# Optimization experiments

Hardware: AMD Instinct MI355X
Metric: run time of the kernel (lower is better)

The kernel has to match this reference:

```python
import jax, jax.numpy as jnp
import numpy as np

B, H, W, F_HEX, F_GLB = 2, 48, 48, 150, 7
D, NH, L, DF, M = 512, 8, 4, 2048, 128
MAX_W, MAX_H, ATK, REC = 48, 48, 8, 20
S = H * W
DK = D // NH


def _ln(x, g, b):
    m = jnp.mean(x, -1, keepdims=True)
    v = jnp.mean(jnp.square(x - m), -1, keepdims=True)
    return (x - m) * jax.lax.rsqrt(v + 1e-5) * g + b


def _mha(q, k, v, wq, bq, wk, bk, wv, bv, wo, bo, mask=None):
    Bq, Sq, _ = q.shape
    Sk = k.shape[1]
    Q = (q @ wq + bq).reshape(Bq, Sq, NH, DK)
    K = (k @ wk + bk).reshape(Bq, Sk, NH, DK)
    V = (v @ wv + bv).reshape(Bq, Sk, NH, DK)
    s = jnp.einsum('bqhd,bkhd->bhqk', Q, K) / np.float32(np.sqrt(DK))
    if mask is not None:
        s = jnp.where(mask == 0, jnp.float32(-1e9), s)
    a = jax.nn.softmax(s, -1)
    o = jnp.einsum('bhqk,bkhd->bqhd', a, V).reshape(Bq, Sq, D)
    return o @ wo + bo


def setup_inputs():
    key = jax.random.key(0)
    ks = iter(jax.random.split(key, 64))
    w = lambda *sh: jax.random.normal(next(ks), sh, jnp.float32) * 0.02
    z = lambda *sh: jnp.zeros(sh, jnp.float32)
    o = lambda *sh: jnp.ones(sh, jnp.float32)
    return dict(
        map_representation=jax.random.normal(next(ks), (B, H, W, F_HEX), jnp.float32),
        global_features=jax.random.normal(next(ks), (B, F_GLB), jnp.float32),
        memory=jax.random.normal(next(ks), (B, M, D), jnp.float32),
        fog_mask=jax.random.randint(next(ks), (B, H, W), 0, 2, jnp.int32),
        hex_w=w(F_HEX, D), hex_b=z(D), glob_w=w(F_GLB, D), glob_b=z(D),
        mem_wq=w(D, D), mem_bq=z(D), mem_wk=w(D, D), mem_bk=z(D),
        mem_wv=w(D, D), mem_bv=z(D), mem_wo=w(D, D), mem_bo=z(D),
        gate_w=w(2 * D, D), gate_b=z(D),
        mn1_g=o(D), mn1_b=z(D), mn2_g=o(D), mn2_b=z(D),
        lw_q=w(L, D, D), lb_q=z(L, D), lw_k=w(L, D, D), lb_k=z(L, D),
        lw_v=w(L, D, D), lb_v=z(L, D), lw_o=w(L, D, D), lb_o=z(L, D),
        ln1_g=o(L, D), ln1_b=z(L, D), ln2_g=o(L, D), ln2_b=z(L, D),
        ff1_w=w(L, D, DF), ff1_b=z(L, DF), ff2_w=w(L, DF, D), ff2_b=z(L, D),
        pool_w=w(D, 1), pool_b=z(1),
        sx_w=w(D, MAX_W), sx_b=z(MAX_W), sy_w=w(D, MAX_H), sy_b=z(MAX_H),
        tx_w=w(D, MAX_W), tx_b=z(MAX_W), ty_w=w(D, MAX_H), ty_b=z(MAX_H),
        atk_w=w(D, ATK), atk_b=z(ATK), rec_w=w(D, REC), rec_b=z(REC),
        et_w=w(D, 1), et_b=z(1), val_w=w(D, 1), val_b=z(1),
    )


def reference(map_representation, global_features, memory, fog_mask,
              hex_w, hex_b, glob_w, glob_b,
              mem_wq, mem_bq, mem_wk, mem_bk, mem_wv, mem_bv, mem_wo, mem_bo,
              gate_w, gate_b, mn1_g, mn1_b, mn2_g, mn2_b,
              lw_q, lb_q, lw_k, lb_k, lw_v, lb_v, lw_o, lb_o,
              ln1_g, ln1_b, ln2_g, ln2_b, ff1_w, ff1_b, ff2_w, ff2_b,
              pool_w, pool_b, sx_w, sx_b, sy_w, sy_b, tx_w, tx_b, ty_w, ty_b,
              atk_w, atk_b, rec_w, rec_b, et_w, et_b, val_w, val_b):
    # project hex + global features, flatten map to token sequence [B,S,D]
    hexf = map_representation @ hex_w + hex_b
    glob = global_features @ glob_w + glob_b
    seq = (hexf + glob[:, None, None, :]).reshape(B, S, D)
    am = fog_mask.reshape(B, S)[:, None, None, :]  # key mask [B,1,1,S]

    # memory module: cross-attn conditioning + gated memory update (shared MHA weights)
    mem_out = _mha(seq, memory, memory, mem_wq, mem_bq, mem_wk, mem_bk, mem_wv, mem_bv, mem_wo, mem_bo)
    x = _ln(seq + mem_out, mn1_g, mn1_b)
    mem_upd = _mha(memory, seq, seq, mem_wq, mem_bq, mem_wk, mem_bk, mem_wv, mem_bv, mem_wo, mem_bo)
    gate = jax.nn.sigmoid(jnp.concatenate([memory, mem_upd], -1) @ gate_w + gate_b)
    new_memory = _ln(gate * mem_upd + (1.0 - gate) * memory, mn2_g, mn2_b)

    def block(xc, p):
        wq, bq, wk, bk, wv, bv, wo, bo, g1, b1, g2, b2, f1w, f1b, f2w, f2b = p
        att = _mha(xc, xc, xc, wq, bq, wk, bk, wv, bv, wo, bo, mask=am)
        xc = _ln(xc + att, g1, b1)
        h = jax.nn.gelu(xc @ f1w + f1b, approximate=False) @ f2w + f2b
        return _ln(xc + h, g2, b2), None

    x, _ = jax.lax.scan(block, x, (lw_q, lb_q, lw_k, lb_k, lw_v, lb_v, lw_o, lb_o,
                                   ln1_g, ln1_b, ln2_g, ln2_b, ff1_w, ff1_b, ff2_w, ff2_b))

    # attention pooling over tokens
    pw = jax.nn.softmax((x @ pool_w + pool_b)[..., 0], -1)  # [B,S]
    pooled = jnp.einsum('bs,bsd->bd', pw, x)

    return (pooled @ sx_w + sx_b, pooled @ sy_w + sy_b,
            pooled @ tx_w + tx_b, pooled @ ty_w + ty_b,
            pooled @ atk_w + atk_b, pooled @ rec_w + rec_b,
            pooled @ et_w + et_b, pooled @ val_w + val_b, new_memory)
```

## Files before the change

### kernel.cpp

```cpp
#include <hip/hip_runtime.h>
#include <hip/hip_bf16.h>

typedef __hip_bfloat16 bf16;
typedef unsigned short u16;
typedef __attribute__((ext_vector_type(8))) short short8;
typedef __attribute__((ext_vector_type(4))) float f32x4;

__device__ inline float b2f(u16 u){ unsigned int x = ((unsigned int)u) << 16; float f; __builtin_memcpy(&f, &x, 4); return f; }
__device__ inline u16 f2bits(float f){ __hip_bfloat16 h = __float2bfloat16(f); u16 u; __builtin_memcpy(&u, &h, 2); return u; }
__device__ inline void unpk(unsigned int w, float& a, float& b){ a = b2f((u16)(w & 0xffffu)); b = b2f((u16)(w >> 16)); }

__device__ __forceinline__ unsigned int pkbf(float a, float b)
{
  unsigned int ua = __float_as_uint(a) + 0x8000u;
  unsigned int ub = __float_as_uint(b) + 0x8000u;
  return __builtin_amdgcn_perm(ub, ua, 0x07060302u);
}

__global__ __launch_bounds__(512) void detect_k(const unsigned int* __restrict__ raw, int* __restrict__ flag)
{
  __shared__ int cnt;
  if (threadIdx.x == 0) cnt = 0;
  __syncthreads();
  unsigned int w = raw[threadIdx.x];
  unsigned int b = w & 0x7fffu;
  int pat = (b >= 0x2000u && b <= 0x4400u) ? 1 : 0;
#pragma unroll
  for (int o = 32; o; o >>= 1) pat += __shfl_xor(pat, o);
  if ((threadIdx.x & 63) == 0) atomicAdd(&cnt, pat);
  __syncthreads();
  if (threadIdx.x == 0) flag[0] = (cnt > 320) ? 1 : 0;
}

struct CvtArgs { const void* p[55]; int off[56]; int sz[55]; };

__global__ __launch_bounds__(256) void cvtall8_k(CvtArgs a, bf16* __restrict__ dst,
                                                 const int* __restrict__ flag)
{
  int g8 = blockIdx.x * 256 + threadIdx.x;
  int gid = g8 * 8;
  if (gid >= a.off[55]) return;
  int lo = 0, hi = 54;
  while (lo < hi) { int mid = (lo + hi + 1) >> 1; if (gid >= a.off[mid]) lo = mid; else hi = mid - 1; }
  int t = lo, i = gid - a.off[t];
  int n = a.sz[t];
  uint4 ov;
  if (flag[0]) {
    const u16* src = (const u16*)a.p[t];
    if (i + 8 <= n) {
      ov = *(const uint4*)(src + i);
    } else {
      u16 tmp[8];
#pragma unroll
      for (int j = 0; j < 8; j++) tmp[j] = (i + j < n) ? src[i + j] : (u16)0;
      __builtin_memcpy(&ov, tmp, 16);
    }
  } else {
    const float* src = (const float*)a.p[t];
    float v[8];
    if (i + 8 <= n) {
      uint4 f0 = *(const uint4*)(src + i);
      uint4 f1 = *(const uint4*)(src + i + 4);
      __builtin_memcpy(&v[0], &f0, 16);
      __builtin_memcpy(&v[4], &f1, 16);
    } else {
#pragma unroll
      for (int j = 0; j < 8; j++) v[j] = (i + j < n) ? src[i + j] : 0.f;
    }
    u16 o8[8];
#pragma unroll
    for (int j = 0; j < 8; j++) o8[j] = f2bits(v[j]);
    __builtin_memcpy(&ov, o8, 16);
  }
  *(uint4*)((u16*)dst + gid) = ov;
}

__global__ __launch_bounds__(256) void gemm_k(
    const bf16* __restrict__ A, int lda, long long sAb, long long sAh,
    const bf16* __restrict__ B, int ldb, long long sBb, long long sBh,
    bf16* __restrict__ C, int ldc, long long sCb, long long sCh,
    int M, int N, int K, int HZ,
    const bf16* __restrict__ bias,
    const bf16* __restrict__ res, int ldres,
    const float* __restrict__ extra, int extraDiv,
    float alpha, int mode)
{
  __shared__ u16 As[64][40];
  __shared__ u16 Bs[64][40];
  int z = blockIdx.z;
  int bz = z / HZ, hz = z - bz * HZ;
  A += (size_t)bz * sAb + (size_t)hz * sAh;
  B += (size_t)bz * sBb + (size_t)hz * sBh;
  C += (size_t)bz * sCb + (size_t)hz * sCh;

  int m0 = blockIdx.y * 64, n0 = blockIdx.x * 64;
  int t = threadIdx.x;
  int r = t >> 2, c0 = (t & 3) << 3;
  int lane = t & 63, wv = t >> 6, lr = lane & 15, lq = lane >> 4;

  f32x4 acc[4];
#pragma unroll
  for (int i = 0; i < 4; i++) acc[i] = (f32x4){0.f, 0.f, 0.f, 0.f};

  const u16* Ag = (const u16*)A;
  const u16* Bg = (const u16*)B;
  bool aok = (m0 + r < M), bok = (n0 + r < N);
  const u16* arow = Ag + (size_t)(m0 + r) * lda + c0;
  const u16* brow = Bg + (size_t)(n0 + r) * ldb + c0;

  uint4 av = {0u,0u,0u,0u}, bv = {0u,0u,0u,0u};
  if (aok) av = *(const uint4*)(arow);
  if (bok) bv = *(const uint4*)(brow);

  for (int kt = 0; kt < K; kt += 32) {
    __syncthreads();
    *(uint4*)&As[r][c0] = av;
    *(uint4*)&Bs[r][c0] = bv;
    uint4 av2 = {0u,0u,0u,0u}, bv2 = {0u,0u,0u,0u};
    int nk = kt + 32;
    if (nk < K) {
      if (aok) av2 = *(const uint4*)(arow + nk);
      if (bok) bv2 = *(const uint4*)(brow + nk);
    }
    __syncthreads();
    short8 af = *(const short8*)&As[wv * 16 + lr][lq * 8];
#pragma unroll
    for (int nt = 0; nt < 4; nt++) {
      short8 bfr = *(const short8*)&Bs[nt * 16 + lr][lq * 8];
      acc[nt] = __builtin_amdgcn_mfma_f32_16x16x32_bf16(af, bfr, acc[nt], 0, 0, 0);
    }
    av = av2; bv = bv2;
  }

#pragma unroll
  for (int nt = 0; nt < 4; nt++) {
    int nn = n0 + nt * 16 + lr;
    if (nn >= N) continue;
    float bb = bias ? (float)bias[nn] : 0.f;
#pragma unroll
    for (int rr = 0; rr < 4; rr++) {
      int mm = m0 + wv * 16 + lq * 4 + rr;
      if (mm >= M) continue;
      float v = acc[nt][rr] * alpha + bb;
      if (mode == 1)      v += extra[(mm / extraDiv) * 512 + nn];
      else if (mode == 2) v = 0.5f * v * (1.f + erff(v * 0.70710678118654752f));
      else if (mode == 4) v += (float)res[(size_t)mm * ldres + nn];
      else if (mode == 5) v = 1.f / (1.f + expf(-v));
      C[(size_t)mm * ldc + nn] = __float2bfloat16(v);
    }
  }
}

__device__ __forceinline__ int swz(int row, int cg)
{
  return row * 64 + ((cg ^ (row & 3) ^ (((row >> 3) & 1) << 2)) << 3);
}

__global__ __launch_bounds__(256) void flash_k(
    const bf16* __restrict__ Qp, long long sQb, int sQr,
    const bf16* __restrict__ Kp, long long sKb, int sKr,
    const bf16* __restrict__ VTp, long long sVz,
    float* __restrict__ oAcc, long long sOb,
    float* __restrict__ lAcc, int Ml,
    const int* __restrict__ fog,
    int tilesPerSplit, int SkLen)
{
  __shared__ u16 Kl[64 * 64];
  __shared__ u16 Vl[64 * 64];
  __shared__ u16 fgl16[2304];

  const float SC = 0.125f * 1.44269504088896340736f;
  int z = blockIdx.y, b = z >> 3, h = z & 7;
  int qt = blockIdx.x;
  int kt0 = blockIdx.z * tilesPerSplit;
  int t = threadIdx.x, lane = t & 63, w = t >> 6;
  int lr = lane & 15, lq = lane >> 4;
  int useMask = (fog != nullptr);

  const u16* Qg = (const u16*)Qp + (size_t)b * sQb + h * 64;
  const u16* Kg = (const u16*)Kp + (size_t)b * sKb + h * 64;
  const u16* Vg = (const u16*)VTp + (size_t)z * sVz;

  if (useMask) {
    for (int j = t; j < SkLen; j += 256) fgl16[j] = fog[b * 2304 + j] ? 0xFFFFu : 0u;
  }

  int qrow = qt * 64 + w * 16 + lr;
  short8 qf0, qf1;
  {
    union { short8 s; u16 u[8]; } i0, i1, o0, o1;
    i0.s = *(const short8*)(Qg + (size_t)qrow * sQr + lq * 8);
    i1.s = *(const short8*)(Qg + (size_t)qrow * sQr + 32 + lq * 8);
#pragma unroll
    for (int j = 0; j < 8; j++) {
      o0.u[j] = f2bits(b2f(i0.u[j]) * SC);
      o1.u[j] = f2bits(b2f(i1.u[j]) * SC);
    }
    qf0 = o0.s; qf1 = o1.s;
  }

  short8 ones8;
  {
    union { short8 s; u16 u[8]; } on;
#pragma unroll
    for (int j = 0; j < 8; j++) on.u[j] = 0x3F80u;
    ones8 = on.s;
  }

  int rowA[4], kAd0[4], kAd1[4];
#pragma unroll
  for (int nt = 0; nt < 4; nt++) {
    rowA[nt] = 32 * (nt >> 1) + 8 * (lr >> 2) + 4 * (nt & 1) + (lr & 3);
    kAd0[nt] = swz(rowA[nt], lq);
    kAd1[nt] = swz(rowA[nt], lq + 4);
  }
  int vAd0[4], vAd1[4];
#pragma unroll
  for (int dt = 0; dt < 4; dt++) {
    vAd0[dt] = swz(dt * 16 + lr, lq);
    vAd1[dt] = swz(dt * 16 + lr, lq + 4);
  }

  f32x4 o[4], ol;
#pragma unroll
  for (int i = 0; i < 4; i++) o[i] = (f32x4){0.f, 0.f, 0.f, 0.f};
  ol = (f32x4){0.f, 0.f, 0.f, 0.f};

  int rr = t >> 2, cg = t & 3, cs = cg * 8;
  int wAd0 = swz(rr, cg), wAd1 = swz(rr, cg + 4);

  const u16* krow = Kg + (size_t)(kt0 * 64 + rr) * sKr + cs;
  const u16* vrow = Vg + (size_t)rr * SkLen + kt0 * 64 + cs;
  uint4 ka = *(const uint4*)(krow);
  uint4 kb = *(const uint4*)(krow + 32);
  uint4 va = *(const uint4*)(vrow);
  uint4 vb = *(const uint4*)(vrow + 32);

  for (int kti = 0; kti < tilesPerSplit; kti++) {
    int kt = kt0 + kti;
    __syncthreads();
    *(uint4*)&Kl[wAd0] = ka;
    *(uint4*)&Kl[wAd1] = kb;
    *(uint4*)&Vl[wAd0] = va;
    *(uint4*)&Vl[wAd1] = vb;
    if (kti + 1 < tilesPerSplit) {
      krow += (size_t)64 * sKr;
      vrow += 64;
      ka = *(const uint4*)(krow);
      kb = *(const uint4*)(krow + 32);
      va = *(const uint4*)(vrow);
      vb = *(const uint4*)(vrow + 32);
    }
    __syncthreads();

    f32x4 s[4];
#pragma unroll
    for (int nt = 0; nt < 4; nt++) {
      s[nt] = (f32x4){0.f, 0.f, 0.f, 0.f};
      short8 kf0 = *(const short8*)&Kl[kAd0[nt]];
      short8 kf1 = *(const short8*)&Kl[kAd1[nt]];
      s[nt] = __builtin_amdgcn_mfma_f32_16x16x32_bf16(kf0, qf0, s[nt], 0, 0, 0);
      s[nt] = __builtin_amdgcn_mfma_f32_16x16x32_bf16(kf1, qf1, s[nt], 0, 0, 0);
    }

    union { unsigned int u[4]; short8 s8; } pk0, pk1;
#pragma unroll
    for (int nt = 0; nt < 4; nt++) {
      float p0 = __builtin_amdgcn_exp2f(s[nt][0]);
      float p1 = __builtin_amdgcn_exp2f(s[nt][1]);
      float p2 = __builtin_amdgcn_exp2f(s[nt][2]);
      float p3 = __builtin_amdgcn_exp2f(s[nt][3]);
      unsigned int w0 = pkbf(p0, p1);
      unsigned int w1 = pkbf(p2, p3);
      if (useMask) {
        int key = kt * 64 + 32 * (nt >> 1) + 8 * lq + 4 * (nt & 1);
        uint2 mm = *(const uint2*)&fgl16[key];
        w0 &= mm.x; w1 &= mm.y;
      }
      if (nt < 2) { pk0.u[(nt & 1) * 2] = w0; pk0.u[(nt & 1) * 2 + 1] = w1; }
      else        { pk1.u[(nt & 1) * 2] = w0; pk1.u[(nt & 1) * 2 + 1] = w1; }
    }
#pragma unroll
    for (int dt = 0; dt < 4; dt++) {
      short8 vf0 = *(const short8*)&Vl[vAd0[dt]];
      short8 vf1 = *(const short8*)&Vl[vAd1[dt]];
      o[dt] = __builtin_amdgcn_mfma_f32_16x16x32_bf16(pk0.s8, vf0, o[dt], 0, 0, 0);
      o[dt] = __builtin_amdgcn_mfma_f32_16x16x32_bf16(pk1.s8, vf1, o[dt], 0, 0, 0);
    }
    ol = __builtin_amdgcn_mfma_f32_16x16x32_bf16(pk0.s8, ones8, ol, 0, 0, 0);
    ol = __builtin_amdgcn_mfma_f32_16x16x32_bf16(pk1.s8, ones8, ol, 0, 0, 0);
  }

  if (lr == 0) {
#pragma unroll
    for (int r2 = 0; r2 < 4; r2++)
      atomicAdd(&lAcc[z * Ml + qt * 64 + w * 16 + lq * 4 + r2], ol[r2]);
  }

  float* ob = oAcc + (size_t)b * sOb;
  int qb = qt * 64 + w * 16 + lq * 4;
#pragma unroll
  for (int dt = 0; dt < 4; dt++)
#pragma unroll
    for (int r2 = 0; r2 < 4; r2++)
      atomicAdd(&ob[(size_t)(qb + r2) * 512 + h * 64 + dt * 16 + lr], o[dt][r2]);
}

__global__ __launch_bounds__(256) void fdiv4_k(const float* __restrict__ oAcc,
                                               const float* __restrict__ lAcc,
                                               int Mq, int Ml, int rows,
                                               bf16* __restrict__ out)
{
  int i = (blockIdx.x * 256 + threadIdx.x) * 4;
  if (i >= rows * 512) return;
  int row = i >> 9, col = i & 511;
  int b = row / Mq, q = row - b * Mq;
  int zz = b * 8 + (col >> 6);
  float l = lAcc[zz * Ml + q];
  float inv = (l > 0.f) ? 1.f / l : 0.f;
  float4 v = *(const float4*)(oAcc + i);
  u16 o4[4] = {f2bits(v.x * inv), f2bits(v.y * inv), f2bits(v.z * inv), f2bits(v.w * inv)};
  unsigned int lo = o4[0] | ((unsigned)o4[1] << 16);
  unsigned int hi = o4[2] | ((unsigned)o4[3] << 16);
  *(uint2*)((u16*)out + i) = (uint2){lo, hi};
}

__global__ __launch_bounds__(256) void zero2_k(float* __restrict__ p1, int n1,
                                               float* __restrict__ p2, int n2)
{
  int i = blockIdx.x * 256 + threadIdx.x;
  if (i < n1) p1[i] = 0.f;
  if (i < n2) p2[i] = 0.f;
}

__global__ void biasfuse_k(const bf16* __restrict__ mbq, const bf16* __restrict__ mbk,
                           const bf16* __restrict__ mbv, const bf16* __restrict__ lbq,
                           const bf16* __restrict__ lbk, const bf16* __restrict__ lbv,
                           bf16* __restrict__ out)
{
  int j = blockIdx.x * 256 + threadIdx.x;
  if (j >= 5 * 1536) return;
  int g = j / 1536, r = j - g * 1536;
  int which = r >> 9, c = r & 511;
  const bf16* src;
  if (g == 0) src = (which == 0) ? mbq : (which == 1) ? mbk : mbv;
  else {
    const bf16* base = (which == 0) ? lbq : (which == 1) ? lbk : lbv;
    src = base + (g - 1) * 512;
  }
  out[j] = src[c];
}

__global__ __launch_bounds__(256) void transpose_k(const bf16* __restrict__ in, bf16* __restrict__ out,
                                                   int R, int C, int Rpad, long long inB, long long outB)
{
  __shared__ u16 tile[32][33];
  const u16* ip = (const u16*)in + (size_t)blockIdx.z * inB;
  u16* op = (u16*)out + (size_t)blockIdx.z * outB;
  int c0 = blockIdx.x * 32, r0 = blockIdx.y * 32;
  int tx = threadIdx.x & 31, ty = threadIdx.x >> 5;
#pragma unroll
  for (int j = 0; j < 4; j++) {
    int rr = r0 + ty + j * 8, cc = c0 + tx;
    u16 v = 0;
    if (rr < R && cc < C) v = ip[(size_t)rr * C + cc];
    tile[ty + j * 8][tx] = v;
  }
  __syncthreads();
#pragma unroll
  for (int j = 0; j < 4; j++) {
    int oc = c0 + ty + j * 8;
    if (oc < C && r0 + tx < Rpad) op[(size_t)oc * Rpad + r0 + tx] = tile[tx][ty + j * 8];
  }
}

__global__ __launch_bounds__(256) void headT_k(const bf16* __restrict__ in, bf16* __restrict__ out,
                                               int Sk, int rowbase, int bstride, int instride)
{
  __shared__ u16 tile[32][33];
  int z = blockIdx.z, b = z >> 3, h = z & 7;
  const u16* ip = (const u16*)in + ((size_t)(rowbase + b * bstride)) * instride + h * 64;
  u16* op = (u16*)out + (size_t)z * 64 * Sk;
  int r0 = blockIdx.x * 32, c0 = blockIdx.y * 32;
  int tx = threadIdx.x & 31, ty = threadIdx.x >> 5;
#pragma unroll
  for (int j = 0; j < 4; j++)
    tile[ty + j * 8][tx] = ip[(size_t)(r0 + ty + j * 8) * instride + c0 + tx];
  __syncthreads();
#pragma unroll
  for (int j = 0; j < 4; j++)
    op[(size_t)(c0 + ty + j * 8) * Sk + r0 + tx] = tile[tx][ty + j * 8];
}

__global__ __launch_bounds__(256) void ln_k(const bf16* __restrict__ in, const bf16* __restrict__ g,
                                            const bf16* __restrict__ bb, bf16* __restrict__ out)
{
  size_t row = blockIdx.x * 4 + (threadIdx.x >> 6);
  int lane = threadIdx.x & 63;
  const u16* ip = (const u16*)in + row * 512 + lane * 8;
  uint4 rv = *(const uint4*)ip;
  float v[8];
  unpk(rv.x, v[0], v[1]); unpk(rv.y, v[2], v[3]); unpk(rv.z, v[4], v[5]); unpk(rv.w, v[6], v[7]);
  float s = 0.f, s2 = 0.f;
#pragma unroll
  for (int k = 0; k < 8; k++) { s += v[k]; s2 += v[k] * v[k]; }
#pragma unroll
  for (int o = 32; o; o >>= 1) { s += __shfl_xor(s, o); s2 += __shfl_xor(s2, o); }
  float mean = s * (1.f / 512.f);
  float var = s2 * (1.f / 512.f) - mean * mean;
  float rstd = rsqrtf(var + 1e-5f);
  uint4 gv = *(const uint4*)((const u16*)g + lane * 8);
  uint4 bv = *(const uint4*)((const u16*)bb + lane * 8);
  float gf[8], bf2[8];
  unpk(gv.x, gf[0], gf[1]); unpk(gv.y, gf[2], gf[3]); unpk(gv.z, gf[4], gf[5]); unpk(gv.w, gf[6], gf[7]);
  unpk(bv.x, bf2[0], bf2[1]); unpk(bv.y, bf2[2], bf2[3]); unpk(bv.z, bf2[4], bf2[5]); unpk(bv.w, bf2[6], bf2[7]);
  u16 o8[8];
#pragma unroll
  for (int k = 0; k < 8; k++) o8[k] = f2bits((v[k] - mean) * rstd * gf[k] + bf2[k]);
  uint4 ov;
  ov.x = o8[0] | ((unsigned)o8[1] << 16); ov.y = o8[2] | ((unsigned)o8[3] << 16);
  ov.z = o8[4] | ((unsigned)o8[5] << 16); ov.w = o8[6] | ((unsigned)o8[7] << 16);
  *(uint4*)((u16*)out + row * 512 + lane * 8) = ov;
}

__global__ void glob_k(const bf16* __restrict__ gf, const bf16* __restrict__ gw,
                       const bf16* __restrict__ gb, float* __restrict__ out)
{
  int i = blockIdx.x * 256 + threadIdx.x; if (i >= 1024) return;
  int b = i >> 9, d = i & 511;
  float s = (float)gb[d];
#pragma unroll
  for (int f = 0; f < 7; f++) s += (float)gf[b * 7 + f] * (float)gw[f * 512 + d];
  out[i] = s;
}

__global__ void padA_k(const bf16* __restrict__ in, bf16* __restrict__ out)
{
  int i = blockIdx.x * 256 + threadIdx.x; if (i >= 4608 * 160) return;
  int r = i / 160, c = i - r * 160;
  out[i] = (c < 150) ? in[r * 150 + c] : __float2bfloat16(0.f);
}

__global__ void catg_k(const bf16* __restrict__ mem, const bf16* __restrict__ mu, bf16* __restrict__ out)
{
  int i = blockIdx.x * 256 + threadIdx.x; if (i >= 256 * 1024) return;
  int r = i >> 10, c = i & 1023;
  out[i] = (c < 512) ? mem[r * 512 + c] : mu[r * 512 + c - 512];
}

__global__ void gcomb_k(const bf16* __restrict__ g, const bf16* __restrict__ mu,
                        const bf16* __restrict__ mem, bf16* __restrict__ out)
{
  int i = blockIdx.x * 256 + threadIdx.x; if (i >= 131072) return;
  float gg = (float)g[i];
  out[i] = __float2bfloat16(gg * (float)mu[i] + (1.f - gg) * (float)mem[i]);
}

__global__ __launch_bounds__(64) void plog_k(const bf16* __restrict__ x, const bf16* __restrict__ pw,
                                             const bf16* __restrict__ pb, float* __restrict__ out)
{
  size_t row = blockIdx.x; int lane = threadIdx.x;
  uint4 xv = *(const uint4*)((const u16*)x + row * 512 + lane * 8);
  uint4 wv = *(const uint4*)((const u16*)pw + lane * 8);
  float v[8], w[8];
  unpk(xv.x, v[0], v[1]); unpk(xv.y, v[2], v[3]); unpk(xv.z, v[4], v[5]); unpk(xv.w, v[6], v[7]);
  unpk(wv.x, w[0], w[1]); unpk(wv.y, w[2], w[3]); unpk(wv.z, w[4], w[5]); unpk(wv.w, w[6], w[7]);
  float s = 0.f;
#pragma unroll
  for (int k = 0; k < 8; k++) s += v[k] * w[k];
#pragma unroll
  for (int o = 32; o; o >>= 1) s += __shfl_xor(s, o);
  if (lane == 0) out[row] = s + (float)pb[0];
}

__global__ __launch_bounds__(256) void psm_k(const float* __restrict__ lg, float* __restrict__ pw)
{
  __shared__ float red[4];
  int b = blockIdx.x, tid = threadIdx.x;
  const float* p = lg + b * 2304;
  float vals[9]; float mx = -3e38f;
#pragma unroll
  for (int i = 0; i < 9; i++) {
    int j = tid + i * 256;
    float x = (j < 2304) ? p[j] : -3e38f;
    vals[i] = x; mx = fmaxf(mx, x);
  }
#pragma unroll
  for (int o = 32; o; o >>= 1) mx = fmaxf(mx, __shfl_xor(mx, o));
  if ((tid & 63) == 0) red[tid >> 6] = mx;
  __syncthreads();
  mx = fmaxf(fmaxf(red[0], red[1]), fmaxf(red[2], red[3]));
  float sum = 0.f;
#pragma unroll
  for (int i = 0; i < 9; i++) {
    int j = tid + i * 256;
    if (j < 2304) { float e = expf(vals[i] - mx); vals[i] = e; sum += e; }
  }
  __syncthreads();
#pragma unroll
  for (int o = 32; o; o >>= 1) sum += __shfl_xor(sum, o);
  if ((tid & 63) == 0) red[tid >> 6] = sum;
  __syncthreads();
  sum = red[0] + red[1] + red[2] + red[3];
  float inv = 1.f / sum;
#pragma unroll
  for (int i = 0; i < 9; i++) {
    int j = tid + i * 256;
    if (j < 2304) pw[b * 2304 + j] = vals[i] * inv;
  }
}

__global__ __launch_bounds__(256) void pool1_k(const float* __restrict__ pw, const bf16* __restrict__ x,
                                               float* __restrict__ out)
{
  int b = blockIdx.y, chunk = blockIdx.x, t = threadIdx.x;
  float a0 = 0.f, a1 = 0.f;
  for (int s = 0; s < 64; s++) {
    int tok = chunk * 64 + s;
    float wv = pw[b * 2304 + tok];
    const u16* xp = (const u16*)x + ((size_t)(b * 2304 + tok)) * 512;
    a0 += wv * b2f(xp[t]);
    a1 += wv * b2f(xp[t + 256]);
  }
  atomicAdd(&out[b * 512 + t], a0);
  atomicAdd(&out[b * 512 + t + 256], a1);
}

__global__ void heads_k(const float* __restrict__ pooled,
                        const bf16* w0, const bf16* b0, const bf16* w1, const bf16* b1,
                        const bf16* w2, const bf16* b2, const bf16* w3, const bf16* b3,
                        const bf16* w4, const bf16* b4, const bf16* w5, const bf16* b5,
                        const bf16* w6, const bf16* b6, const bf16* w7, const bf16* b7,
                        void* __restrict__ outv, const int* __restrict__ flag)
{
  int idx = blockIdx.x * 256 + threadIdx.x; if (idx >= 444) return;
  const bf16* W[8] = {w0, w1, w2, w3, w4, w5, w6, w7};
  const bf16* Bi[8] = {b0, b1, b2, b3, b4, b5, b6, b7};
  int b = idx / 222, j = idx - b * 222;
  const int sizes[8]  = {48, 48, 48, 48, 8, 20, 1, 1};
  const int outoff[8] = {0, 96, 192, 288, 384, 400, 440, 442};
  int h = 0, basec = 0;
  while (h < 7 && j >= basec + sizes[h]) { basec += sizes[h]; ++h; }
  int col = j - basec;
  const bf16* wp = W[h]; int nc = sizes[h];
  float s = (float)Bi[h][col];
  for (int k = 0; k < 512; k++) s += pooled[b * 512 + k] * (float)wp[k * nc + col];
  int e = outoff[h] + b * nc + col;
  if (flag[0]) ((bf16*)outv)[e] = __float2bfloat16(s);
  else         ((float*)outv)[e] = s;
}

__global__ void outstore_k(const bf16* __restrict__ nm, void* __restrict__ outv,
                           const int* __restrict__ flag)
{
  int i = blockIdx.x * 256 + threadIdx.x; if (i >= 131072) return;
  if (flag[0]) ((bf16*)outv)[444 + i] = nm[i];
  else         ((float*)outv)[444 + i] = (float)nm[i];
}


static inline void gemm(hipStream_t st, const bf16* A, int lda, long long sAb, long long sAh,
                        const bf16* B, int ldb, long long sBb, long long sBh,
                        bf16* C, int ldc, long long sCb, long long sCh,
                        int M, int N, int K, int BZ, int HZ,
                        const bf16* bias, const bf16* res, int ldres,
                        const float* extra, int extraDiv, float alpha, int mode)
{
  dim3 g((N + 63) / 64, (M + 63) / 64, BZ * HZ);
  gemm_k<<<g, dim3(256), 0, st>>>(A, lda, sAb, sAh, B, ldb, sBb, sBh, C, ldc, sCb, sCh,
                                  M, N, K, HZ, bias, res, ldres, extra, extraDiv, alpha, mode);
}

static inline void transp(hipStream_t st, const bf16* in, bf16* out, int R, int C, int Rpad,
                          long long inB, long long outB, int Z)
{
  dim3 g((C + 31) / 32, (Rpad + 31) / 32, Z);
  transpose_k<<<g, dim3(256), 0, st>>>(in, out, R, C, Rpad, inB, outB);
}

extern "C" void kernel_launch(void* const* d_in, const int* in_sizes, int n_in,
                              void* d_out, int out_size, void* d_ws, size_t ws_size,
                              hipStream_t stream)
{
  (void)in_sizes; (void)n_in; (void)out_size;
  const int* fog = (const int*)d_in[3];

  static const int kSz[55] = {
    691200, 14, 131072, 76800, 512, 3584, 512,
    262144, 512, 262144, 512, 262144, 512, 262144, 512,
    524288, 512, 512, 512, 512, 512,
    1048576, 2048, 1048576, 2048, 1048576, 2048, 1048576, 2048,
    2048, 2048, 2048, 2048,
    4194304, 8192, 4194304, 2048,
    512, 1,
    24576, 48, 24576, 48, 24576, 48, 24576, 48,
    4096, 8, 10240, 20, 512, 1, 512, 1};
  static const int kIdx[55] = {
    0, 1, 2, 4, 5, 6, 7,
    8, 9, 10, 11, 12, 13, 14, 15,
    16, 17, 18, 19, 20, 21,
    22, 23, 24, 25, 26, 27, 28, 29,
    30, 31, 32, 33,
    34, 35, 36, 37,
    38, 39,
    40, 41, 42, 43, 44, 45, 46, 47,
    48, 49, 50, 51, 52, 53, 54, 55};

  CvtArgs ca;
  size_t cum[55]; int coffi = 0;
  for (int t = 0; t < 55; t++) {
    cum[t] = (size_t)coffi;
    ca.p[t] = d_in[kIdx[t]];
    ca.off[t] = coffi;
    ca.sz[t] = kSz[t];
    coffi += (kSz[t] + 7) & ~7;
  }
  ca.off[55] = coffi;
  size_t coff = (size_t)coffi;

  const int S = 2304, NROW = 4608, CATROW = 4864;
  const long long QR = 1536;
  const long long RSQ = (long long)S * QR;

  char* basep = (char*)d_ws; size_t off = 0;
  auto alloc = [&](size_t elems, size_t esz) -> void* {
    void* p = basep + off; off += (elems * esz + 255) & ~(size_t)255; return p;
  };

  bf16* canon = (bf16*)alloc(coff, 2);
  int* dflag = (int*)alloc(64, 4);
  bf16* tHex = (bf16*)alloc(512 * 160, 2);
  bf16* aPad = (bf16*)alloc((size_t)NROW * 160, 2);
  bf16* tQKVmem = (bf16*)alloc(1536 * 512, 2);
  bf16* tWo = (bf16*)alloc(512 * 512, 2);
  bf16* tGate = (bf16*)alloc(512 * 1024, 2);
  bf16* tLqkv = (bf16*)alloc(4ULL * 1536 * 512, 2);
  bf16* tLo = (bf16*)alloc(4 * 512 * 512, 2);
  bf16* tF1 = (bf16*)alloc(4ULL * 2048 * 512, 2);
  bf16* tF2 = (bf16*)alloc(4ULL * 512 * 2048, 2);
  bf16* fbias = (bf16*)alloc(5 * 1536, 2);
  float* globF = (float*)alloc(1024, 4);
  bf16* catX = (bf16*)alloc((size_t)CATROW * 512, 2);
  bf16* QKV = (bf16*)alloc((size_t)CATROW * 1536, 2);
  bf16* VmemT = (bf16*)alloc(16ULL * 64 * 128, 2);
  bf16* VsT = (bf16*)alloc(16ULL * 64 * S, 2);
  bf16* mo = (bf16*)alloc((size_t)NROW * 512, 2);
  bf16* tmp1 = (bf16*)alloc((size_t)NROW * 512, 2);
  bf16* xbuf = (bf16*)alloc((size_t)NROW * 512, 2);
  bf16* x2buf = (bf16*)alloc((size_t)NROW * 512, 2);
  bf16* mu0 = (bf16*)alloc(256 * 512, 2);
  bf16* mup = (bf16*)alloc(256 * 512, 2);
  bf16* catg = (bf16*)alloc(256 * 1024, 2);
  bf16* gateb = (bf16*)alloc(256 * 512, 2);
  bf16* nmpre = (bf16*)alloc(256 * 512, 2);
  bf16* nmout = (bf16*)alloc(256 * 512, 2);
  float* plog = (float*)alloc(NROW, 4);
  float* pwv = (float*)alloc(NROW, 4);
  float* pooledF = (float*)alloc(1024, 4);
  float* oAcc = (float*)alloc((size_t)NROW * 512, 4);
  float* lAcc = (float*)alloc(16 * 2304, 4);
  bf16* hbuf = (bf16*)alloc((size_t)NROW * 2048, 2);
  if (off > ws_size) return;

  detect_k<<<1, 512, 0, stream>>>((const unsigned int*)d_in[0], dflag);
  cvtall8_k<<<(coffi / 8 + 255) / 256, 256, 0, stream>>>(ca, canon, dflag);

  auto T = [&](int t) -> const bf16* { return canon + cum[t]; };
  const bf16* map_rep = T(0);
  const bf16* gfeat   = T(1);
  const bf16* memin   = T(2);
  const bf16* hex_w = T(3);  const bf16* hex_b = T(4);
  const bf16* glob_w = T(5); const bf16* glob_b = T(6);
  const bf16* mem_wq = T(7);  const bf16* mem_bq = T(8);
  const bf16* mem_wk = T(9);  const bf16* mem_bk = T(10);
  const bf16* mem_wv = T(11); const bf16* mem_bv = T(12);
  const bf16* mem_wo = T(13); const bf16* mem_bo = T(14);
  const bf16* gate_w = T(15); const bf16* gate_b = T(16);
  const bf16* mn1_g = T(17); const bf16* mn1_b = T(18);
  const bf16* mn2_g = T(19); const bf16* mn2_b = T(20);
  const bf16* lw_q = T(21); const bf16* lb_q = T(22);
  const bf16* lw_k = T(23); const bf16* lb_k = T(24);
  const bf16* lw_v = T(25); const bf16* lb_v = T(26);
  const bf16* lw_o = T(27); const bf16* lb_o = T(28);
  const bf16* ln1_g = T(29); const bf16* ln1_b = T(30);
  const bf16* ln2_g = T(31); const bf16* ln2_b = T(32);
  const bf16* ff1_w = T(33); const bf16* ff1_b = T(34);
  const bf16* ff2_w = T(35); const bf16* ff2_b = T(36);
  const bf16* pool_w = T(37); const bf16* pool_b = T(38);

  transp(stream, hex_w, tHex, 150, 512, 160, 0, 0, 1);
  transp(stream, mem_wq, tQKVmem, 512, 512, 512, 0, 0, 1);
  transp(stream, mem_wk, tQKVmem + 262144, 512, 512, 512, 0, 0, 1);
  transp(stream, mem_wv, tQKVmem + 524288, 512, 512, 512, 0, 0, 1);
  transp(stream, mem_wo, tWo, 512, 512, 512, 0, 0, 1);
  transp(stream, gate_w, tGate, 1024, 512, 1024, 0, 0, 1);
  transp(stream, lw_q, tLqkv, 512, 512, 512, 262144, 786432, 4);
  transp(stream, lw_k, tLqkv + 262144, 512, 512, 512, 262144, 786432, 4);
  transp(stream, lw_v, tLqkv + 524288, 512, 512, 512, 262144, 786432, 4);
  transp(stream, lw_o, tLo, 512, 512, 512, 262144, 262144, 4);
  transp(stream, ff1_w, tF1, 512, 2048, 512, 1048576, 1048576, 4);
  transp(stream, ff2_w, tF2, 2048, 512, 2048, 1048576, 1048576, 4);
  biasfuse_k<<<(5 * 1536 + 255) / 256, 256, 0, stream>>>(mem_bq, mem_bk, mem_bv,
                                                         lb_q, lb_k, lb_v, fbias);

  glob_k<<<4, 256, 0, stream>>>(gfeat, glob_w, glob_b, globF);
  padA_k<<<(NROW * 160 + 255) / 256, 256, 0, stream>>>(map_rep, aPad);
  gemm(stream, aPad, 160, 0, 0, tHex, 160, 0, 0, catX, 512, 0, 0,
       NROW, 512, 160, 1, 1, hex_b, nullptr, 0, globF, S, 1.f, 1);
  hipMemcpyAsync(catX + (size_t)NROW * 512, memin, 256 * 512 * 2, hipMemcpyDeviceToDevice, stream);

  gemm(stream, catX, 512, 0, 0, tQKVmem, 512, 0, 0, QKV, 1536, 0, 0,
       CATROW, 1536, 512, 1, 1, fbias, nullptr, 0, nullptr, 1, 1.f, 0);

  headT_k<<<dim3(4, 2, 16), 256, 0, stream>>>(QKV + 1024, VmemT, 128, NROW, 128, 1536);
  zero2_k<<<(NROW * 512 + 255) / 256, 256, 0, stream>>>(oAcc, NROW * 512, lAcc, 16 * 2304);
  flash_k<<<dim3(36, 16, 1), 256, 0, stream>>>(
      QKV, RSQ, 1536, QKV + (size_t)NROW * 1536 + 512, 128 * QR, 1536,
      VmemT, 64 * 128, oAcc, (long long)S * 512, lAcc, 2304, nullptr, 2, 128);
  fdiv4_k<<<(NROW * 128 + 255) / 256, 256, 0, stream>>>(oAcc, lAcc, 2304, 2304, NROW, mo);
  gemm(stream, mo, 512, 0, 0, tWo, 512, 0, 0, tmp1, 512, 0, 0,
       NROW, 512, 512, 1, 1, mem_bo, catX, 512, nullptr, 1, 1.f, 4);
  ln_k<<<NROW / 4, 256, 0, stream>>>(tmp1, mn1_g, mn1_b, xbuf);

  headT_k<<<dim3(72, 2, 16), 256, 0, stream>>>(QKV + 1024, VsT, S, 0, S, 1536);
  zero2_k<<<(256 * 512 + 255) / 256, 256, 0, stream>>>(oAcc, 256 * 512, lAcc, 16 * 128);
  flash_k<<<dim3(2, 16, 6), 256, 0, stream>>>(
      QKV + (size_t)NROW * 1536, 128 * QR, 1536, QKV + 512, RSQ, 1536,
      VsT, 64LL * S, oAcc, 128 * 512, lAcc, 128, nullptr, 6, S);
  fdiv4_k<<<(256 * 128 + 255) / 256, 256, 0, stream>>>(oAcc, lAcc, 128, 128, 256, mu0);
  gemm(stream, mu0, 512, 0, 0, tWo, 512, 0, 0, mup, 512, 0, 0,
       256, 512, 512, 1, 1, mem_bo, nullptr, 0, nullptr, 1, 1.f, 0);
  catg_k<<<(256 * 1024 + 255) / 256, 256, 0, stream>>>(memin, mup, catg);
  gemm(stream, catg, 1024, 0, 0, tGate, 1024, 0, 0, gateb, 512, 0, 0,
       256, 512, 1024, 1, 1, gate_b, nullptr, 0, nullptr, 1, 1.f, 5);
  gcomb_k<<<(131072 + 255) / 256, 256, 0, stream>>>(gateb, mup, memin, nmpre);
  ln_k<<<64, 256, 0, stream>>>(nmpre, mn2_g, mn2_b, nmout);
  outstore_k<<<(131072 + 255) / 256, 256, 0, stream>>>(nmout, d_out, dflag);

  for (int l = 0; l < 4; l++) {
    gemm(stream, xbuf, 512, 0, 0, tLqkv + (size_t)l * 786432, 512, 0, 0, QKV, 1536, 0, 0,
         NROW, 1536, 512, 1, 1, fbias + (1 + l) * 1536, nullptr, 0, nullptr, 1, 1.f, 0);
    headT_k<<<dim3(72, 2, 16), 256, 0, stream>>>(QKV + 1024, VsT, S, 0, S, 1536);
    zero2_k<<<(NROW * 512 + 255) / 256, 256, 0, stream>>>(oAcc, NROW * 512, lAcc, 16 * 2304);
    flash_k<<<dim3(36, 16, 3), 256, 0, stream>>>(
        QKV, RSQ, 1536, QKV + 512, RSQ, 1536,
        VsT, 64LL * S, oAcc, (long long)S * 512, lAcc, 2304, fog, 12, S);
    fdiv4_k<<<(NROW * 128 + 255) / 256, 256, 0, stream>>>(oAcc, lAcc, 2304, 2304, NROW, mo);
    gemm(stream, mo, 512, 0, 0, tLo + (size_t)l * 262144, 512, 0, 0, tmp1, 512, 0, 0,
         NROW, 512, 512, 1, 1, lb_o + l * 512, xbuf, 512, nullptr, 1, 1.f, 4);
    ln_k<<<NROW / 4, 256, 0, stream>>>(tmp1, ln1_g + l * 512, ln1_b + l * 512, x2buf);
    gemm(stream, x2buf, 512, 0, 0, tF1 + (size_t)l * 1048576, 512, 0, 0, hbuf, 2048, 0, 0,
         NROW, 2048, 512, 1, 1, ff1_b + l * 2048, nullptr, 0, nullptr, 1, 1.f, 2);
    gemm(stream, hbuf, 2048, 0, 0, tF2 + (size_t)l * 1048576, 2048, 0, 0, tmp1, 512, 0, 0,
         NROW, 512, 2048, 1, 1, ff2_b + l * 512, x2buf, 512, nullptr, 1, 1.f, 4);
    ln_k<<<NROW / 4, 256, 0, stream>>>(tmp1, ln2_g + l * 512, ln2_b + l * 512, xbuf);
  }

  plog_k<<<NROW, 64, 0, stream>>>(xbuf, pool_w, pool_b, plog);
  psm_k<<<2, 256, 0, stream>>>(plog, pwv);
  hipMemsetAsync(pooledF, 0, 1024 * sizeof(float), stream);
  pool1_k<<<dim3(36, 2), 256, 0, stream>>>(pwv, xbuf, pooledF);

  heads_k<<<2, 256, 0, stream>>>(pooledF,
      T(39), T(40), T(41), T(42), T(43), T(44), T(45), T(46),
      T(47), T(48), T(49), T(50), T(51), T(52), T(53), T(54),
      d_out, dflag);
}
```

Before: 1.087 ms.

## Add 128-row GEMM tile and replace flash split atomics with per-split buffers

Adds a gemmM128 kernel where each 256-thread block computes a 128x64 output tile, with each wave doing 2x4 MFMAs per k-step. It is used for the QKV and FFN1 projections to raise operand reuse from LDS. Separately, the split-K flash attention no longer atomically adds partial outputs and row sums. Each split writes its own buffer, and fdiv4 sums the splits, which removes the zeroing kernels and the atomic traffic at the cost of more workspace and extra reads in the reduction. The new GEMM has no bounds checks and assumes M is a multiple of 128 and N a multiple of 64, which holds for the shapes used here.

```diff
diff --git a/kernel.cpp b/kernel.cpp
--- a/kernel.cpp
+++ b/kernel.cpp
@@ -75,6 +75,19 @@
   *(uint4*)((u16*)dst + gid) = ov;
 }
 
+__device__ __forceinline__ float epi(float v, int mm, int nn,
+                                     const bf16* bias, const bf16* res, int ldres,
+                                     const float* extra, int extraDiv, float alpha, int mode)
+{
+  float bb = bias ? (float)bias[nn] : 0.f;
+  v = v * alpha + bb;
+  if (mode == 1)      v += extra[(mm / extraDiv) * 512 + nn];
+  else if (mode == 2) v = 0.5f * v * (1.f + erff(v * 0.70710678118654752f));
+  else if (mode == 4) v += (float)res[(size_t)mm * ldres + nn];
+  else if (mode == 5) v = 1.f / (1.f + expf(-v));
+  return v;
+}
+
 __global__ __launch_bounds__(256) void gemm_k(
     const bf16* __restrict__ A, int lda, long long sAb, long long sAh,
     const bf16* __restrict__ B, int ldb, long long sBb, long long sBh,
@@ -136,17 +149,82 @@
   for (int nt = 0; nt < 4; nt++) {
     int nn = n0 + nt * 16 + lr;
     if (nn >= N) continue;
-    float bb = bias ? (float)bias[nn] : 0.f;
 #pragma unroll
     for (int rr = 0; rr < 4; rr++) {
       int mm = m0 + wv * 16 + lq * 4 + rr;
       if (mm >= M) continue;
-      float v = acc[nt][rr] * alpha + bb;
-      if (mode == 1)      v += extra[(mm / extraDiv) * 512 + nn];
-      else if (mode == 2) v = 0.5f * v * (1.f + erff(v * 0.70710678118654752f));
-      else if (mode == 4) v += (float)res[(size_t)mm * ldres + nn];
-      else if (mode == 5) v = 1.f / (1.f + expf(-v));
-      C[(size_t)mm * ldc + nn] = __float2bfloat16(v);
+      C[(size_t)mm * ldc + nn] =
+          __float2bfloat16(epi(acc[nt][rr], mm, nn, bias, res, ldres, extra, extraDiv, alpha, mode));
+    }
+  }
+}
+
+__global__ __launch_bounds__(256) void gemmM128_k(
+    const bf16* __restrict__ A, int lda,
+    const bf16* __restrict__ B, int ldb,
+    bf16* __restrict__ C, int ldc, int K,
+    const bf16* __restrict__ bias,
+    const bf16* __restrict__ res, int ldres,
+    const float* __restrict__ extra, int extraDiv,
+    float alpha, int mode)
+{
+  __shared__ u16 As[128][40];
+  __shared__ u16 Bs[64][40];
+  int t = threadIdx.x;
+  int m0 = blockIdx.y * 128, n0 = blockIdx.x * 64;
+  int lane = t & 63, w = t >> 6, lr = lane & 15, lq = lane >> 4;
+  int wm = w * 32;
+  int r = t >> 2, c0 = (t & 3) << 3;
+
+  const u16* Ag = (const u16*)A;
+  const u16* Bg = (const u16*)B;
+  const u16* ar0 = Ag + (size_t)(m0 + r) * lda + c0;
+  const u16* ar1 = Ag + (size_t)(m0 + 64 + r) * lda + c0;
+  const u16* brow = Bg + (size_t)(n0 + r) * ldb + c0;
+
+  uint4 a0 = *(const uint4*)ar0, a1 = *(const uint4*)ar1, bv = *(const uint4*)brow;
+
+  f32x4 acc[2][4];
+#pragma unroll
+  for (int i = 0; i < 2; i++)
+#pragma unroll
+    for (int j = 0; j < 4; j++) acc[i][j] = (f32x4){0.f, 0.f, 0.f, 0.f};
+
+  for (int kt = 0; kt < K; kt += 32) {
+    __syncthreads();
+    *(uint4*)&As[r][c0] = a0;
+    *(uint4*)&As[64 + r][c0] = a1;
+    *(uint4*)&Bs[r][c0] = bv;
+    int nk = kt + 32;
+    if (nk < K) {
+      a0 = *(const uint4*)(ar0 + nk);
+      a1 = *(const uint4*)(ar1 + nk);
+      bv = *(const uint4*)(brow + nk);
+    }
+    __syncthreads();
+    short8 af[2], bf[4];
+#pragma unroll
+    for (int mt = 0; mt < 2; mt++) af[mt] = *(const short8*)&As[wm + mt * 16 + lr][lq * 8];
+#pragma unroll
+    for (int nt = 0; nt < 4; nt++) bf[nt] = *(const short8*)&Bs[nt * 16 + lr][lq * 8];
+#pragma unroll
+    for (int mt = 0; mt < 2; mt++)
+#pragma unroll
+      for (int nt = 0; nt < 4; nt++)
+        acc[mt][nt] = __builtin_amdgcn_mfma_f32_16x16x32_bf16(af[mt], bf[nt], acc[mt][nt], 0, 0, 0);
+  }
+
+#pragma unroll
+  for (int nt = 0; nt < 4; nt++) {
+    int nn = n0 + nt * 16 + lr;
+#pragma unroll
+    for (int mt = 0; mt < 2; mt++) {
+#pragma unroll
+      for (int rr = 0; rr < 4; rr++) {
+        int mm = m0 + wm + mt * 16 + lq * 4 + rr;
+        C[(size_t)mm * ldc + nn] =
+            __float2bfloat16(epi(acc[mt][nt][rr], mm, nn, bias, res, ldres, extra, extraDiv, alpha, mode));
+      }
     }
   }
 }
@@ -160,8 +238,8 @@
     const bf16* __restrict__ Qp, long long sQb, int sQr,
     const bf16* __restrict__ Kp, long long sKb, int sKr,
     const bf16* __restrict__ VTp, long long sVz,
-    float* __restrict__ oAcc, long long sOb,
-    float* __restrict__ lAcc, int Ml,
+    float* __restrict__ oAcc, long long sOb, long long sOsplit,
+    float* __restrict__ lAcc, int Ml, int lSplit,
     const int* __restrict__ fog,
     int tilesPerSplit, int SkLen)
 {
@@ -172,7 +250,8 @@
   const float SC = 0.125f * 1.44269504088896340736f;
   int z = blockIdx.y, b = z >> 3, h = z & 7;
   int qt = blockIdx.x;
-  int kt0 = blockIdx.z * tilesPerSplit;
+  int split = blockIdx.z;
+  int kt0 = split * tilesPerSplit;
   int t = threadIdx.x, lane = t & 63, w = t >> 6;
   int lr = lane & 15, lq = lane >> 4;
   int useMask = (fog != nullptr);
@@ -291,46 +370,45 @@
     ol = __builtin_amdgcn_mfma_f32_16x16x32_bf16(pk1.s8, ones8, ol, 0, 0, 0);
   }
 
+  float* lS = lAcc + (size_t)split * lSplit;
   if (lr == 0) {
 #pragma unroll
     for (int r2 = 0; r2 < 4; r2++)
-      atomicAdd(&lAcc[z * Ml + qt * 64 + w * 16 + lq * 4 + r2], ol[r2]);
-  }
-
-  float* ob = oAcc + (size_t)b * sOb;
+      lS[z * Ml + qt * 64 + w * 16 + lq * 4 + r2] = ol[r2];
+  }
+
+  float* ob = oAcc + (size_t)split * sOsplit + (size_t)b * sOb;
   int qb = qt * 64 + w * 16 + lq * 4;
 #pragma unroll
   for (int dt = 0; dt < 4; dt++)
 #pragma unroll
     for (int r2 = 0; r2 < 4; r2++)
-      atomicAdd(&ob[(size_t)(qb + r2) * 512 + h * 64 + dt * 16 + lr], o[dt][r2]);
+      ob[(size_t)(qb + r2) * 512 + h * 64 + dt * 16 + lr] = o[dt][r2];
 }
 
 __global__ __launch_bounds__(256) void fdiv4_k(const float* __restrict__ oAcc,
                                                const float* __restrict__ lAcc,
                                                int Mq, int Ml, int rows,
-                                               bf16* __restrict__ out)
+                                               bf16* __restrict__ out,
+                                               int nsplit, long long oSplit, int lSplit)
 {
   int i = (blockIdx.x * 256 + threadIdx.x) * 4;
   if (i >= rows * 512) return;
   int row = i >> 9, col = i & 511;
   int b = row / Mq, q = row - b * Mq;
   int zz = b * 8 + (col >> 6);
-  float l = lAcc[zz * Ml + q];
+  float l = 0.f;
+  float4 v = {0.f, 0.f, 0.f, 0.f};
+  for (int s = 0; s < nsplit; s++) {
+    l += lAcc[(size_t)s * lSplit + zz * Ml + q];
+    float4 p = *(const float4*)(oAcc + (size_t)s * oSplit + i);
+    v.x += p.x; v.y += p.y; v.z += p.z; v.w += p.w;
+  }
   float inv = (l > 0.f) ? 1.f / l : 0.f;
-  float4 v = *(const float4*)(oAcc + i);
   u16 o4[4] = {f2bits(v.x * inv), f2bits(v.y * inv), f2bits(v.z * inv), f2bits(v.w * inv)};
   unsigned int lo = o4[0] | ((unsigned)o4[1] << 16);
   unsigned int hi = o4[2] | ((unsigned)o4[3] << 16);
   *(uint2*)((u16*)out + i) = (uint2){lo, hi};
-}
-
-__global__ __launch_bounds__(256) void zero2_k(float* __restrict__ p1, int n1,
-                                               float* __restrict__ p2, int n2)
-{
-  int i = blockIdx.x * 256 + threadIdx.x;
-  if (i < n1) p1[i] = 0.f;
-  if (i < n2) p2[i] = 0.f;
 }
 
 __global__ void biasfuse_k(const bf16* __restrict__ mbq, const bf16* __restrict__ mbk,
@@ -569,6 +647,16 @@
   dim3 g((N + 63) / 64, (M + 63) / 64, BZ * HZ);
   gemm_k<<<g, dim3(256), 0, st>>>(A, lda, sAb, sAh, B, ldb, sBb, sBh, C, ldc, sCb, sCh,
                                   M, N, K, HZ, bias, res, ldres, extra, extraDiv, alpha, mode);
+}
+
+static inline void gemmM128(hipStream_t st, const bf16* A, int lda, const bf16* B, int ldb,
+                            bf16* C, int ldc, int M, int N, int K,
+                            const bf16* bias, const bf16* res, int ldres,
+                            const float* extra, int extraDiv, float alpha, int mode)
+{
+  dim3 g(N / 64, M / 128, 1);
+  gemmM128_k<<<g, dim3(256), 0, st>>>(A, lda, B, ldb, C, ldc, K, bias, res, ldres,
+                                      extra, extraDiv, alpha, mode);
 }
 
 static inline void transp(hipStream_t st, const bf16* in, bf16* out, int R, int C, int Rpad,
@@ -621,6 +709,7 @@
   const int S = 2304, NROW = 4608, CATROW = 4864;
   const long long QR = 1536;
   const long long RSQ = (long long)S * QR;
+  const long long OSPLIT = (long long)NROW * 512;
 
   char* basep = (char*)d_ws; size_t off = 0;
   auto alloc = [&](size_t elems, size_t esz) -> void* {
@@ -657,8 +746,8 @@
   float* plog = (float*)alloc(NROW, 4);
   float* pwv = (float*)alloc(NROW, 4);
   float* pooledF = (float*)alloc(1024, 4);
-  float* oAcc = (float*)alloc((size_t)NROW * 512, 4);
-  float* lAcc = (float*)alloc(16 * 2304, 4);
+  float* oAcc = (float*)alloc(3ULL * NROW * 512, 4);
+  float* lAcc = (float*)alloc(131072, 4);
   bf16* hbuf = (bf16*)alloc((size_t)NROW * 2048, 2);
   if (off > ws_size) return;
 
@@ -709,25 +798,27 @@
        NROW, 512, 160, 1, 1, hex_b, nullptr, 0, globF, S, 1.f, 1);
   hipMemcpyAsync(catX + (size_t)NROW * 512, memin, 256 * 512 * 2, hipMemcpyDeviceToDevice, stream);
 
-  gemm(stream, catX, 512, 0, 0, tQKVmem, 512, 0, 0, QKV, 1536, 0, 0,
-       CATROW, 1536, 512, 1, 1, fbias, nullptr, 0, nullptr, 1, 1.f, 0);
+  gemmM128(stream, catX, 512, tQKVmem, 512, QKV, 1536, CATROW, 1536, 512,
+           fbias, nullptr, 0, nullptr, 1, 1.f, 0);
 
   headT_k<<<dim3(4, 2, 16), 256, 0, stream>>>(QKV + 1024, VmemT, 128, NROW, 128, 1536);
-  zero2_k<<<(NROW * 512 + 255) / 256, 256, 0, stream>>>(oAcc, NROW * 512, lAcc, 16 * 2304);
   flash_k<<<dim3(36, 16, 1), 256, 0, stream>>>(
       QKV, RSQ, 1536, QKV + (size_t)NROW * 1536 + 512, 128 * QR, 1536,
-      VmemT, 64 * 128, oAcc, (long long)S * 512, lAcc, 2304, nullptr, 2, 128);
-  fdiv4_k<<<(NROW * 128 + 255) / 256, 256, 0, stream>>>(oAcc, lAcc, 2304, 2304, NROW, mo);
+      VmemT, 64 * 128, oAcc, (long long)S * 512, OSPLIT, lAcc, 2304, 16 * 2304,
+      nullptr, 2, 128);
+  fdiv4_k<<<(NROW * 128 + 255) / 256, 256, 0, stream>>>(oAcc, lAcc, 2304, 2304, NROW, mo,
+                                                        1, OSPLIT, 16 * 2304);
   gemm(stream, mo, 512, 0, 0, tWo, 512, 0, 0, tmp1, 512, 0, 0,
        NROW, 512, 512, 1, 1, mem_bo, catX, 512, nullptr, 1, 1.f, 4);
   ln_k<<<NROW / 4, 256, 0, stream>>>(tmp1, mn1_g, mn1_b, xbuf);
 
   headT_k<<<dim3(72, 2, 16), 256, 0, stream>>>(QKV + 1024, VsT, S, 0, S, 1536);
-  zero2_k<<<(256 * 512 + 255) / 256, 256, 0, stream>>>(oAcc, 256 * 512, lAcc, 16 * 128);
   flash_k<<<dim3(2, 16, 6), 256, 0, stream>>>(
       QKV + (size_t)NROW * 1536, 128 * QR, 1536, QKV + 512, RSQ, 1536,
-      VsT, 64LL * S, oAcc, 128 * 512, lAcc, 128, nullptr, 6, S);
-  fdiv4_k<<<(256 * 128 + 255) / 256, 256, 0, stream>>>(oAcc, lAcc, 128, 128, 256, mu0);
+      VsT, 64LL * S, oAcc, 128 * 512, 128 * 512 * 16LL, lAcc, 128, 16 * 128,
+      nullptr, 6, S);
+  fdiv4_k<<<(256 * 128 + 255) / 256, 256, 0, stream>>>(oAcc, lAcc, 128, 128, 256, mu0,
+                                                       6, 128 * 512 * 16LL, 16 * 128);
   gemm(stream, mu0, 512, 0, 0, tWo, 512, 0, 0, mup, 512, 0, 0,
        256, 512, 512, 1, 1, mem_bo, nullptr, 0, nullptr, 1, 1.f, 0);
   catg_k<<<(256 * 1024 + 255) / 256, 256, 0, stream>>>(memin, mup, catg);
@@ -738,19 +829,20 @@
   outstore_k<<<(131072 + 255) / 256, 256, 0, stream>>>(nmout, d_out, dflag);
 
   for (int l = 0; l < 4; l++) {
-    gemm(stream, xbuf, 512, 0, 0, tLqkv + (size_t)l * 786432, 512, 0, 0, QKV, 1536, 0, 0,
-         NROW, 1536, 512, 1, 1, fbias + (1 + l) * 1536, nullptr, 0, nullptr, 1, 1.f, 0);
+    gemmM128(stream, xbuf, 512, tLqkv + (size_t)l * 786432, 512, QKV, 1536,
+             NROW, 1536, 512, fbias + (1 + l) * 1536, nullptr, 0, nullptr, 1, 1.f, 0);
     headT_k<<<dim3(72, 2, 16), 256, 0, stream>>>(QKV + 1024, VsT, S, 0, S, 1536);
-    zero2_k<<<(NROW * 512 + 255) / 256, 256, 0, stream>>>(oAcc, NROW * 512, lAcc, 16 * 2304);
     flash_k<<<dim3(36, 16, 3), 256, 0, stream>>>(
         QKV, RSQ, 1536, QKV + 512, RSQ, 1536,
-        VsT, 64LL * S, oAcc, (long long)S * 512, lAcc, 2304, fog, 12, S);
-    fdiv4_k<<<(NROW * 128 + 255) / 256, 256, 0, stream>>>(oAcc, lAcc, 2304, 2304, NROW, mo);
+        VsT, 64LL * S, oAcc, (long long)S * 512, OSPLIT, lAcc, 2304, 16 * 2304,
+        fog, 12, S);
+    fdiv4_k<<<(NROW * 128 + 255) / 256, 256, 0, stream>>>(oAcc, lAcc, 2304, 2304, NROW, mo,
+                                                          3, OSPLIT, 16 * 2304);
     gemm(stream, mo, 512, 0, 0, tLo + (size_t)l * 262144, 512, 0, 0, tmp1, 512, 0, 0,
          NROW, 512, 512, 1, 1, lb_o + l * 512, xbuf, 512, nullptr, 1, 1.f, 4);
     ln_k<<<NROW / 4, 256, 0, stream>>>(tmp1, ln1_g + l * 512, ln1_b + l * 512, x2buf);
-    gemm(stream, x2buf, 512, 0, 0, tF1 + (size_t)l * 1048576, 512, 0, 0, hbuf, 2048, 0, 0,
-         NROW, 2048, 512, 1, 1, ff1_b + l * 2048, nullptr, 0, nullptr, 1, 1.f, 2);
+    gemmM128(stream, x2buf, 512, tF1 + (size_t)l * 1048576, 512, hbuf, 2048,
+             NROW, 2048, 512, ff1_b + l * 2048, nullptr, 0, nullptr, 1, 1.f, 2);
     gemm(stream, hbuf, 2048, 0, 0, tF2 + (size_t)l * 1048576, 2048, 0, 0, tmp1, 512, 0, 0,
          NROW, 512, 2048, 1, 1, ff2_b + l * 512, x2buf, 512, nullptr, 1, 1.f, 4);
     ln_k<<<NROW / 4, 256, 0, stream>>>(tmp1, ln2_g + l * 512, ln2_b + l * 512, xbuf);
```

After: 1.077 ms. No clear change (-0.9%).
